# Kernel optimization log

Measured on AMD Instinct MI355X. Metric: run time of the kernel, lower is better.

## Reference

```python
import jax, jax.numpy as jnp
import numpy as np

K_SIZE = 5


def _extract_patches(x, k):
    """x: [n, b, h, w, c] -> [n, b, h, w, k*k, c] with zero SAME padding.

    Matches tf.image.extract_patches row-major patch ordering with channels
    fastest, as consumed by the Reshape((H, W, k*k, Ci)) in the original.
    """
    p = k // 2
    n, b, h, w, c = x.shape
    xp = jnp.pad(x, ((0, 0), (0, 0), (p, p), (p, p), (0, 0)))
    shifts = [xp[:, :, i:i + h, j:j + w, :] for i in range(k) for j in range(k)]
    return jnp.stack(shifts, axis=4)


def setup_inputs() -> dict:
    key = jax.random.key(0)
    k1, k2, k3, k4 = jax.random.split(key, 4)
    B, H, W, C = 4, 128, 128, 64
    heads, Ci = 4, 16  # intermediate_dim=64, head_num=4
    main = jax.random.normal(k1, (B, H, W, C), jnp.float32)
    ref = jax.random.normal(k2, (B, H, W, C), jnp.float32)
    he_std = np.sqrt(2.0 / C).astype(np.float32)  # he_normal, fan_in=C (1x1 conv)
    w_main = jax.random.normal(k3, (heads, C, Ci), jnp.float32) * he_std
    w_ref = jax.random.normal(k4, (heads, C, Ci), jnp.float32) * he_std
    return {"main": main, "ref": ref, "w_main": w_main, "w_ref": w_ref}


def reference(main, ref, w_main, w_ref):
    # per-head 1x1 convs (no bias): [n,b,h,w,d]
    q = jnp.einsum('bhwc,ncd->nbhwd', main, w_main)
    r = jnp.einsum('bhwc,ncd->nbhwd', ref, w_ref)
    patches = _extract_patches(r, K_SIZE)          # [n,b,h,w,k*k,d]
    attn = jnp.einsum('nbhwd,nbhwkd->nbhwk', q, patches)
    attn = jax.nn.softmax(attn, axis=-1)           # softmax over k*k neighbors
    return jnp.mean(attn, axis=0)                  # average over heads -> [b,h,w,k*k]
```

## Files before the change

### kernel.cpp

```cpp
#include <hip/hip_runtime.h>
#include <hip/hip_bf16.h>

typedef _Float16 f16;
typedef f16 f16x2 __attribute__((ext_vector_type(2)));
typedef f16 f16x4 __attribute__((ext_vector_type(4)));
typedef f16 f16x8 __attribute__((ext_vector_type(8)));
typedef float f32x4 __attribute__((ext_vector_type(4)));

constexpr int B_  = 4;
constexpr int H_  = 128;
constexpr int W_  = 128;
constexpr int C_  = 64;
constexpr int NH_ = 4;
constexpr int D_  = 16;
constexpr int KK_ = 25;

constexpr int TW_  = 8, TH_ = 8;
constexpr int HWID = 12, HHEI = 12;
constexpr int NPX  = HHEI * HWID;
constexpr int MOFF  = NPX * 64 * 2;
constexpr int MSOFF = 27648;
constexpr int SMEM  = 31744;
constexpr int PSTRIDE = KK_ + 2;
constexpr int PSLAB   = 64 * PSTRIDE;

#if __has_builtin(__builtin_amdgcn_fdot2)
#define FDOT2(a, b, c) __builtin_amdgcn_fdot2((a), (b), (c), false)
#else
#define FDOT2(a, b, c) fmaf((float)(a)[1], (float)(b)[1], fmaf((float)(a)[0], (float)(b)[0], (c)))
#endif

__device__ __forceinline__ int div12(int x) { return (x * 171) >> 11; }

__global__ __launch_bounds__(512, 8) void rl8mh15(
    const float* __restrict__ mainp, const float* __restrict__ refp,
    const float* __restrict__ wmain, const float* __restrict__ wref,
    float* __restrict__ out)
{
    __shared__ __align__(16) unsigned char smraw[SMEM];
    f16*    abuf  = (f16*)smraw;
    f16*    mabuf = (f16*)(smraw + MOFF);
    float*  xbuf  = (float*)smraw;
    float2* msbuf = (float2*)(smraw + MSOFF);

    const int tid = threadIdx.x;
    const int l   = tid & 63;
    const int wid = __builtin_amdgcn_readfirstlane(tid >> 6);
    const int n   = wid & 3;
    const int h   = wid >> 2;
    const int row = l & 15;
    const int kg  = l >> 4;

    const int bid = blockIdx.y * 16 + blockIdx.x;
    const int swz = (bid & 7) * 32 + (bid >> 3);
    const int x0 = (swz & 15) * TW_;
    const int y0 = (swz >> 4) * TH_;
    const int b  = blockIdx.z;
    const float* mainb = mainp + ((size_t)b * H_) * W_ * C_;
    const float* refb  = refp  + ((size_t)b * H_) * W_ * C_;

    for (int j = tid; j < NPX * 16; j += 512) {
        int hp = j >> 4, c4 = j & 15;
        int hy = div12(hp), hx = hp - hy * HWID;
        int gy = y0 + hy - 2, gx = x0 + hx - 2;
        float4 v = make_float4(0.f, 0.f, 0.f, 0.f);
        if ((unsigned)gy < (unsigned)H_ && (unsigned)gx < (unsigned)W_)
            v = *(const float4*)(refb + ((size_t)gy * W_ + gx) * C_ + c4 * 4);
        f16x4 h4 = {(f16)v.x, (f16)v.y, (f16)v.z, (f16)v.w};
        int off = hp * 64 + ((((c4 >> 1) ^ (hp & 7)) << 3) | ((c4 & 1) << 2));
        *(f16x4*)(abuf + off) = h4;
    }
    for (int j = tid; j < 64 * 16; j += 512) {
        int px = j >> 4, c4 = j & 15;
        int gy = y0 + (px >> 3), gx = x0 + (px & 7);
        float4 v = *(const float4*)(mainb + ((size_t)gy * W_ + gx) * C_ + c4 * 4);
        f16x4 h4 = {(f16)v.x, (f16)v.y, (f16)v.z, (f16)v.w};
        int off = px * 64 + ((((c4 >> 1) ^ (px & 7)) << 3) | ((c4 & 1) << 2));
        *(f16x4*)(mabuf + off) = h4;
    }
    __syncthreads();

    auto build_w = [&](const float* wsrc, f16x8* A) {
        const float* w = wsrc + n * C_ * D_;
        #pragma unroll
        for (int s = 0; s < 2; ++s) {
            union { f16x8 v; f16 e[8]; } u;
            #pragma unroll
            for (int i = 0; i < 8; ++i)
                u.e[i] = (f16)w[(s * 32 + kg * 8 + i) * D_ + row];
            A[s] = u.v;
        }
    };

    auto proj = [&](const f16* src, int t, const f16x8* A) -> f16x4 {
        int px = t * 16 + row;
        const f16* rp = src + px * 64;
        f16x8 B0 = *(const f16x8*)(rp + (((kg     ^ (px & 7)) << 3)));
        f16x8 B1 = *(const f16x8*)(rp + ((((kg+4) ^ (px & 7)) << 3)));
        f32x4 acc = {0.f, 0.f, 0.f, 0.f};
        acc = __builtin_amdgcn_mfma_f32_16x16x32_f16(A[0], B0, acc, 0, 0, 0);
        acc = __builtin_amdgcn_mfma_f32_16x16x32_f16(A[1], B1, acc, 0, 0, 0);
        return f16x4{(f16)acc[0], (f16)acc[1], (f16)acc[2], (f16)acc[3]};
    };
    f16x4 racc0, racc1, racc2, racc3, racc4, qacc0, qacc1;
    {
        f16x8 ar[2];
        build_w(wref, ar);
        if (h == 0) {
            racc0 = proj(abuf, 0, ar); racc1 = proj(abuf, 2, ar);
            racc2 = proj(abuf, 4, ar); racc3 = proj(abuf, 6, ar);
            racc4 = proj(abuf, 8, ar);
        } else {
            racc0 = proj(abuf, 1, ar); racc1 = proj(abuf, 3, ar);
            racc2 = proj(abuf, 5, ar); racc3 = proj(abuf, 7, ar);
        }
    }
    {
        f16x8 am[2];
        build_w(wmain, am);
        if (h == 0) { qacc0 = proj(mabuf, 0, am); qacc1 = proj(mabuf, 2, am); }
        else        { qacc0 = proj(mabuf, 1, am); qacc1 = proj(mabuf, 3, am); }
    }
    __syncthreads();

    auto wrout = [&](f16* dst, int t, f16x4 v) {
        int px = t * 16 + row;
        int c16 = (n << 1) | (kg >> 1);
        int off = px * 64 + (((c16 ^ (px & 7)) << 3) | ((kg & 1) << 2));
        *(f16x4*)(dst + off) = v;
    };
    if (h == 0) {
        wrout(abuf, 0, racc0); wrout(abuf, 2, racc1); wrout(abuf, 4, racc2);
        wrout(abuf, 6, racc3); wrout(abuf, 8, racc4);
        wrout(mabuf, 0, qacc0); wrout(mabuf, 2, qacc1);
    } else {
        wrout(abuf, 1, racc0); wrout(abuf, 3, racc1); wrout(abuf, 5, racc2);
        wrout(abuf, 7, racc3);
        wrout(mabuf, 1, qacc0); wrout(mabuf, 3, qacc1);
    }
    __syncthreads();

    const int py  = l >> 3;
    const int pxx = l & 7;
    f16x8 q0 = *(const f16x8*)(mabuf + l * 64 + ((((n << 1) | 0) ^ (l & 7)) << 3));
    f16x8 q1 = *(const f16x8*)(mabuf + l * 64 + ((((n << 1) | 1) ^ (l & 7)) << 3));
    const f16x2* q2a = (const f16x2*)&q0;
    const f16x2* q2b = (const f16x2*)&q1;

    float lg[13];
    auto do_lg = [&](int idx, int k) {
        int ky = k / 5, kx = k % 5;
        int np = (py + ky) * 12 + pxx + kx;
        const f16* rp = abuf + np * 64;
        f16x8 r0 = *(const f16x8*)(rp + ((((n << 1) | 0) ^ (np & 7)) << 3));
        f16x8 r1 = *(const f16x8*)(rp + ((((n << 1) | 1) ^ (np & 7)) << 3));
        const f16x2* r2a = (const f16x2*)&r0;
        const f16x2* r2b = (const f16x2*)&r1;
        float a = 0.f;
        #pragma unroll
        for (int j = 0; j < 4; ++j) a = FDOT2(q2a[j], r2a[j], a);
        #pragma unroll
        for (int j = 0; j < 4; ++j) a = FDOT2(q2b[j], r2b[j], a);
        lg[idx] = a;
    };
    if (h == 0) {
        do_lg(0,0);  do_lg(1,1);  do_lg(2,2);  do_lg(3,3);  do_lg(4,4);
        do_lg(5,5);  do_lg(6,6);  do_lg(7,7);  do_lg(8,8);  do_lg(9,9);
        do_lg(10,10); do_lg(11,11); do_lg(12,12);
    } else {
        do_lg(0,13); do_lg(1,14); do_lg(2,15); do_lg(3,16); do_lg(4,17);
        do_lg(5,18); do_lg(6,19); do_lg(7,20); do_lg(8,21); do_lg(9,22);
        do_lg(10,23); do_lg(11,24);
        lg[12] = -1e30f;
    }

    float mloc = lg[0];
    #pragma unroll
    for (int k = 1; k < 13; ++k) mloc = fmaxf(mloc, lg[k]);

    float s = 0.f;
    f16x2 pk[7];
    #pragma unroll
    for (int j = 0; j < 6; ++j) {
        float e0 = __expf(lg[2*j]   - mloc);
        float e1 = __expf(lg[2*j+1] - mloc);
        s += e0 + e1;
        pk[j] = f16x2{(f16)e0, (f16)e1};
    }
    {
        float e12 = __expf(lg[12] - mloc);
        s += e12;
        pk[6] = f16x2{(f16)e12, (f16)0.f};
    }
    msbuf[(h * 4 + n) * 64 + l] = make_float2(mloc, s);
    __syncthreads();
    float2 o = msbuf[((1 - h) * 4 + n) * 64 + l];
    float m    = fmaxf(mloc, o.x);
    float sc   = __expf(mloc - m);
    float osc  = __expf(o.x  - m);
    float inv  = sc / (s * sc + o.y * osc);

    {
        float* dst = &xbuf[n * PSLAB + l * PSTRIDE + h * 13];
        #pragma unroll
        for (int j = 0; j < 6; ++j) {
            dst[2*j]     = (float)pk[j][0] * inv;
            dst[2*j + 1] = (float)pk[j][1] * inv;
        }
        if (h == 0) dst[12] = (float)pk[6][0] * inv;
    }
    __syncthreads();

    for (int i = tid; i < TW_ * TH_ * KK_; i += 512) {
        int p2 = i / KK_;
        int k  = i - p2 * KK_;
        int off = p2 * PSTRIDE + k;
        float v = 0.25f * (xbuf[off] + xbuf[PSLAB + off] + xbuf[2 * PSLAB + off] + xbuf[3 * PSLAB + off]);
        out[(((size_t)b * H_ + (y0 + (p2 >> 3))) * W_ + (x0 + (p2 & 7))) * KK_ + k] = v;
    }
}

extern "C" void kernel_launch(void* const* d_in, const int* in_sizes, int n_in,
                              void* d_out, int out_size, void* d_ws, size_t ws_size,
                              hipStream_t stream) {
    const float* mainp = (const float*)d_in[0];
    const float* refp  = (const float*)d_in[1];
    const float* wmain = (const float*)d_in[2];
    const float* wref  = (const float*)d_in[3];
    float* outp = (float*)d_out;

    dim3 grid(W_ / TW_, H_ / TH_, B_);
    rl8mh15<<<grid, dim3(512), 0, stream>>>(mainp, refp, wmain, wref, outp);
}
```

Measured before the change: 19.23 us.

## Split softmax halves within a wavefront and merge via lane shuffle

Remaps the logit stage so each wavefront handles 32 pixels, with its two lane halves covering overlapping halves of the 25 neighbours (0-12 and 12-24). The cross-half softmax merge becomes a __shfl_xor across 32 lanes, which removes one block-wide barrier and the LDS exchange buffer. The normalized probabilities are now stored in a separate fp16 LDS region instead of an aliased fp32 one, cutting LDS traffic but adding fp16 rounding to the head average. The overlapping neighbour is computed twice, and the lane-half softmax sum has to exclude it.

```diff
diff --git a/kernel.cpp b/kernel.cpp
--- a/kernel.cpp
+++ b/kernel.cpp
@@ -19,10 +19,10 @@
 constexpr int HWID = 12, HHEI = 12;
 constexpr int NPX  = HHEI * HWID;
 constexpr int MOFF  = NPX * 64 * 2;
-constexpr int MSOFF = 27648;
-constexpr int SMEM  = 31744;
-constexpr int PSTRIDE = KK_ + 2;
-constexpr int PSLAB   = 64 * PSTRIDE;
+constexpr int POFF  = MOFF + 64 * 64 * 2;
+constexpr int PSTR  = KK_ + 1;
+constexpr int PSLAB = 64 * PSTR;
+constexpr int SMEM  = POFF + NH_ * PSLAB * 2;
 
 #if __has_builtin(__builtin_amdgcn_fdot2)
 #define FDOT2(a, b, c) __builtin_amdgcn_fdot2((a), (b), (c), false)
@@ -31,17 +31,17 @@
 #endif
 
 __device__ __forceinline__ int div12(int x) { return (x * 171) >> 11; }
-
-__global__ __launch_bounds__(512, 8) void rl8mh15(
+__device__ __forceinline__ int div5(int x)  { return (x * 205) >> 10; }
+
+__global__ __launch_bounds__(512, 8) void rl8mh16(
     const float* __restrict__ mainp, const float* __restrict__ refp,
     const float* __restrict__ wmain, const float* __restrict__ wref,
     float* __restrict__ out)
 {
     __shared__ __align__(16) unsigned char smraw[SMEM];
-    f16*    abuf  = (f16*)smraw;
-    f16*    mabuf = (f16*)(smraw + MOFF);
-    float*  xbuf  = (float*)smraw;
-    float2* msbuf = (float2*)(smraw + MSOFF);
+    f16* abuf  = (f16*)smraw;
+    f16* mabuf = (f16*)(smraw + MOFF);
+    f16* pxbuf = (f16*)(smraw + POFF);
 
     const int tid = threadIdx.x;
     const int l   = tid & 63;
@@ -140,16 +140,23 @@
     }
     __syncthreads();
 
-    const int py  = l >> 3;
-    const int pxx = l & 7;
-    f16x8 q0 = *(const f16x8*)(mabuf + l * 64 + ((((n << 1) | 0) ^ (l & 7)) << 3));
-    f16x8 q1 = *(const f16x8*)(mabuf + l * 64 + ((((n << 1) | 1) ^ (l & 7)) << 3));
+    const int pbase = (wid >> 2) * 32;
+    const int px  = pbase + (l & 31);
+    const int hh  = l >> 5;
+    const int py  = px >> 3;
+    const int pxx = px & 7;
+
+    f16x8 q0 = *(const f16x8*)(mabuf + px * 64 + ((((n << 1) | 0) ^ (px & 7)) << 3));
+    f16x8 q1 = *(const f16x8*)(mabuf + px * 64 + ((((n << 1) | 1) ^ (px & 7)) << 3));
     const f16x2* q2a = (const f16x2*)&q0;
     const f16x2* q2b = (const f16x2*)&q1;
 
     float lg[13];
-    auto do_lg = [&](int idx, int k) {
-        int ky = k / 5, kx = k % 5;
+    #pragma unroll
+    for (int j = 0; j < 13; ++j) {
+        int k  = hh * 12 + j;
+        int ky = div5(k);
+        int kx = k - 5 * ky;
         int np = (py + ky) * 12 + pxx + kx;
         const f16* rp = abuf + np * 64;
         f16x8 r0 = *(const f16x8*)(rp + ((((n << 1) | 0) ^ (np & 7)) << 3));
@@ -158,64 +165,41 @@
         const f16x2* r2b = (const f16x2*)&r1;
         float a = 0.f;
         #pragma unroll
-        for (int j = 0; j < 4; ++j) a = FDOT2(q2a[j], r2a[j], a);
-        #pragma unroll
-        for (int j = 0; j < 4; ++j) a = FDOT2(q2b[j], r2b[j], a);
-        lg[idx] = a;
-    };
-    if (h == 0) {
-        do_lg(0,0);  do_lg(1,1);  do_lg(2,2);  do_lg(3,3);  do_lg(4,4);
-        do_lg(5,5);  do_lg(6,6);  do_lg(7,7);  do_lg(8,8);  do_lg(9,9);
-        do_lg(10,10); do_lg(11,11); do_lg(12,12);
-    } else {
-        do_lg(0,13); do_lg(1,14); do_lg(2,15); do_lg(3,16); do_lg(4,17);
-        do_lg(5,18); do_lg(6,19); do_lg(7,20); do_lg(8,21); do_lg(9,22);
-        do_lg(10,23); do_lg(11,24);
-        lg[12] = -1e30f;
+        for (int jj = 0; jj < 4; ++jj) a = FDOT2(q2a[jj], r2a[jj], a);
+        #pragma unroll
+        for (int jj = 0; jj < 4; ++jj) a = FDOT2(q2b[jj], r2b[jj], a);
+        lg[j] = a;
     }
 
     float mloc = lg[0];
     #pragma unroll
-    for (int k = 1; k < 13; ++k) mloc = fmaxf(mloc, lg[k]);
-
+    for (int j = 1; j < 13; ++j) mloc = fmaxf(mloc, lg[j]);
     float s = 0.f;
-    f16x2 pk[7];
     #pragma unroll
-    for (int j = 0; j < 6; ++j) {
-        float e0 = __expf(lg[2*j]   - mloc);
-        float e1 = __expf(lg[2*j+1] - mloc);
-        s += e0 + e1;
-        pk[j] = f16x2{(f16)e0, (f16)e1};
-    }
+    for (int j = 0; j < 13; ++j) { lg[j] = __expf(lg[j] - mloc); s += lg[j]; }
+    float s_own = hh ? (s - lg[0]) : s;
+    float om = __shfl_xor(mloc, 32);
+    float os = __shfl_xor(s_own, 32);
+    float m   = fmaxf(mloc, om);
+    float sc  = __expf(mloc - m);
+    float osc = __expf(om - m);
+    float inv = sc / (s_own * sc + os * osc);
+
     {
-        float e12 = __expf(lg[12] - mloc);
-        s += e12;
-        pk[6] = f16x2{(f16)e12, (f16)0.f};
-    }
-    msbuf[(h * 4 + n) * 64 + l] = make_float2(mloc, s);
-    __syncthreads();
-    float2 o = msbuf[((1 - h) * 4 + n) * 64 + l];
-    float m    = fmaxf(mloc, o.x);
-    float sc   = __expf(mloc - m);
-    float osc  = __expf(o.x  - m);
-    float inv  = sc / (s * sc + o.y * osc);
-
-    {
-        float* dst = &xbuf[n * PSLAB + l * PSTRIDE + h * 13];
-        #pragma unroll
-        for (int j = 0; j < 6; ++j) {
-            dst[2*j]     = (float)pk[j][0] * inv;
-            dst[2*j + 1] = (float)pk[j][1] * inv;
-        }
-        if (h == 0) dst[12] = (float)pk[6][0] * inv;
+        f16* dst = pxbuf + n * PSLAB + px * PSTR + hh * 12;
+        #pragma unroll
+        for (int j = 0; j < 13; ++j) dst[j] = (f16)(lg[j] * inv);
     }
     __syncthreads();
 
     for (int i = tid; i < TW_ * TH_ * KK_; i += 512) {
         int p2 = i / KK_;
         int k  = i - p2 * KK_;
-        int off = p2 * PSTRIDE + k;
-        float v = 0.25f * (xbuf[off] + xbuf[PSLAB + off] + xbuf[2 * PSLAB + off] + xbuf[3 * PSLAB + off]);
+        int off = p2 * PSTR + k;
+        float v = 0.25f * ((float)pxbuf[off]
+                         + (float)pxbuf[PSLAB + off]
+                         + (float)pxbuf[2 * PSLAB + off]
+                         + (float)pxbuf[3 * PSLAB + off]);
         out[(((size_t)b * H_ + (y0 + (p2 >> 3))) * W_ + (x0 + (p2 & 7))) * KK_ + k] = v;
     }
 }
@@ -230,5 +214,5 @@
     float* outp = (float*)d_out;
 
     dim3 grid(W_ / TW_, H_ / TH_, B_);
-    rl8mh15<<<grid, dim3(512), 0, stream>>>(mainp, refp, wmain, wref, outp);
+    rl8mh16<<<grid, dim3(512), 0, stream>>>(mainp, refp, wmain, wref, outp);
 }
```

Measured after the change: 19.88 us. 1.03x slower.
